# Performance work log

Hardware: AMD Instinct MI355X
Metric: run time of the kernel (lower is better)

Reference implementation:

```python
import jax, jax.numpy as jnp
import numpy as np

N_DATA = 1200000
FEAT = 128
BATCH = 512
N_NEG = 4096
TEMP = 0.07
MOMENTUM = 0.5


def _l2norm(x):
    return x / jnp.maximum(jnp.linalg.norm(x, axis=-1, keepdims=True), 1e-12)


def setup_inputs() -> dict:
    key = jax.random.key(0)
    k1, k2, k3, k4, k5 = jax.random.split(key, 5)
    negatives = _l2norm(jax.random.normal(k1, (N_DATA, FEAT), dtype=jnp.float32))
    return {
        "student_feat": jax.random.normal(k2, (BATCH, FEAT), dtype=jnp.float32),
        "teacher_feat": jax.random.normal(k3, (BATCH, FEAT), dtype=jnp.float32),
        "negatives": negatives,
        "indices": jax.random.randint(k4, (BATCH,), 0, N_DATA, dtype=jnp.int64)
            if jax.config.read("jax_enable_x64") else jax.random.randint(k4, (BATCH,), 0, N_DATA, dtype=jnp.int32),
        "neg_indices": jax.random.randint(k5, (BATCH, N_NEG), 0, N_DATA, dtype=jnp.int32),
    }


def reference(student_feat, teacher_feat, negatives, indices, neg_indices):
    s = _l2norm(student_feat)                       # [B, D]
    t = _l2norm(teacher_feat)                       # [B, D]
    pos_sim = jnp.sum(s * t, axis=1) / TEMP         # [B]
    neg_feat = negatives[neg_indices]               # [B, K, D] gather from bank
    neg_sim = jnp.einsum('bd,bkd->bk', s, neg_feat) / TEMP  # [B, K]
    logits = jnp.concatenate([pos_sim[:, None], neg_sim], axis=1)  # [B, 1+K]
    # cross-entropy with label 0 for every row
    loss = jnp.mean(jax.nn.logsumexp(logits, axis=1) - logits[:, 0])
    # EMA scatter update + renormalize of touched rows (no-grad side effect)
    upd = MOMENTUM * negatives[indices] + (1.0 - MOMENTUM) * t
    upd = _l2norm(upd)
    new_negatives = negatives.at[indices].set(upd)
    return loss, new_negatives
```

## Files before the change

### kernel.cpp

```cpp
#include <hip/hip_runtime.h>

constexpr int   FEAT   = 128;
constexpr int   BATCH  = 512;
constexpr int   NNEG   = 4096;
constexpr long  NDATA  = 1200000;
constexpr int   CHUNKS = 8;
constexpr int   NCOPY  = 1024;
constexpr long  NSRCG  = NDATA * FEAT / 4;
constexpr long  GMAXO  = NSRCG;
constexpr float INV_TEMP = 14.285714285714286f;
constexpr float LOG2E    = 1.4426950408889634f;
constexpr float LN2      = 0.6931471805599453f;
constexpr float K1       = INV_TEMP * LOG2E;

typedef float f4 __attribute__((ext_vector_type(4)));

__global__ __launch_bounds__(128) void prep_kernel(
    const float* __restrict__ sf, const float* __restrict__ tf,
    float* __restrict__ s_n, float* __restrict__ t_n, float* __restrict__ pos) {
  const int b = blockIdx.x, t = threadIdx.x;
  const float sv = sf[b * FEAT + t];
  const float tv = tf[b * FEAT + t];
  float ss = sv * sv, tt = tv * tv, st = sv * tv;
#pragma unroll
  for (int m = 1; m < 64; m <<= 1) {
    ss += __shfl_xor(ss, m);
    tt += __shfl_xor(tt, m);
    st += __shfl_xor(st, m);
  }
  __shared__ float sh[6];
  if ((t & 63) == 0) {
    const int w = t >> 6;
    sh[w * 3 + 0] = ss; sh[w * 3 + 1] = tt; sh[w * 3 + 2] = st;
  }
  __syncthreads();
  ss = sh[0] + sh[3]; tt = sh[1] + sh[4]; st = sh[2] + sh[5];
  const float snorm = fmaxf(sqrtf(ss), 1e-12f);
  const float tnorm = fmaxf(sqrtf(tt), 1e-12f);
  s_n[b * FEAT + t] = sv / snorm;
  t_n[b * FEAT + t] = tv / tnorm;
  if (t == 0) pos[b] = st / (snorm * tnorm) * INV_TEMP;
}

__global__ __launch_bounds__(256) void work_kernel(
    const float* __restrict__ neg, const int* __restrict__ nidx,
    const float* __restrict__ s_n, float* __restrict__ sumexp,
    float* __restrict__ out) {
  if (blockIdx.x < NCOPY) {
    const long n = NDATA * (long)FEAT;
    const f4* __restrict__ ps = (const f4*)neg;
    f4* __restrict__ po = (f4*)out;
    if (blockIdx.x == 0 && threadIdx.x == 0) {
      out[1] = neg[0]; out[2] = neg[1]; out[3] = neg[2];
      out[n] = neg[n - 1];
    }
    const int lane = threadIdx.x & 63;
    const int wid  = blockIdx.x * 4 + (threadIdx.x >> 6);
    constexpr long NWAVE = (long)NCOPY * 4;
    constexpr long PER   = (GMAXO - 1 + NWAVE - 1) / NWAVE;
    long base = 1 + (long)wid * PER;
    const long gend = (base + PER < GMAXO) ? base + PER : GMAXO;
    if (base >= gend) return;
    long src = base - 1 + lane;
    f4 cur = ps[src < NSRCG ? src : NSRCG - 1];
    while (base < gend) {
      const long nbase = base + 63;
      f4 nxt = {0.f, 0.f, 0.f, 0.f};
      if (nbase < gend) {
        const long ns = nbase - 1 + lane;
        nxt = ps[ns < NSRCG ? ns : NSRCG - 1];
      }
      const float pw = __shfl_up(cur.w, 1);
      const long g = base + lane - 1;
      if (lane >= 1 && g < gend) {
        f4 v; v.x = pw; v.y = cur.x; v.z = cur.y; v.w = cur.z;
        __builtin_nontemporal_store(v, po + g);
      }
      cur = nxt;
      base = nbase;
    }
    return;
  }
  __shared__ float part[4];
  const int blk   = blockIdx.x - NCOPY;
  const int b     = blk >> 3;
  const int chunk = blk & (CHUNKS - 1);
  const int t     = threadIdx.x;
  const int lane  = t & 63;
  const int w     = t >> 6;
  const int half  = lane >> 5;
  const int fo    = (lane & 31) * 4;
  const f4 s4 = *(const f4*)(s_n + b * FEAT + fo);
  const int kbase = b * NNEG + chunk * (NNEG / CHUNKS) + w * 128;
  float acc = 0.f;
  int off[8];
#pragma unroll
  for (int u = 0; u < 8; ++u)
    off[u] = nidx[kbase + 2 * u + half] * FEAT;
  for (int k0 = 0; k0 < 128; k0 += 16) {
    int noff[8];
    if (k0 + 16 < 128) {
#pragma unroll
      for (int u = 0; u < 8; ++u)
        noff[u] = nidx[kbase + k0 + 16 + 2 * u + half] * FEAT;
    }
    f4 v[8];
#pragma unroll
    for (int u = 0; u < 8; ++u)
      v[u] = *(const f4*)(neg + (long)off[u] + fo);
    float p[8];
#pragma unroll
    for (int u = 0; u < 8; ++u) {
      const f4 m = v[u] * s4;
      p[u] = (m.x + m.y) + (m.z + m.w);
    }
#pragma unroll
    for (int ms = 1; ms <= 16; ms <<= 1) {
#pragma unroll
      for (int u = 0; u < 8; ++u) p[u] += __shfl_xor(p[u], ms);
    }
#pragma unroll
    for (int u = 0; u < 8; ++u) acc += exp2f(fmaf(p[u], K1, -K1));
#pragma unroll
    for (int u = 0; u < 8; ++u) off[u] = noff[u];
  }
  acc *= (1.0f / 32.0f);
#pragma unroll
  for (int m = 1; m < 64; m <<= 1) acc += __shfl_xor(acc, m);
  if (lane == 0) part[w] = acc;
  __syncthreads();
  if (t == 0)
    sumexp[blk] = part[0] + part[1] + part[2] + part[3];
}

__global__ __launch_bounds__(256) void finish_kernel(
    const float* __restrict__ pos, const float* __restrict__ sumexp,
    const float* __restrict__ neg, const float* __restrict__ t_n,
    const int* __restrict__ indices, float* __restrict__ out) {
  const int t = threadIdx.x;
  if (blockIdx.x == 0) {
    float lsum = 0.f;
#pragma unroll
    for (int r = t; r < BATCH; r += 256) {
      const float p = pos[r];
      float tot = exp2f(fmaf(p, LOG2E, -K1));
#pragma unroll
      for (int c = 0; c < CHUNKS; ++c) tot += sumexp[r * CHUNKS + c];
      lsum += INV_TEMP + log2f(tot) * LN2 - p;
    }
#pragma unroll
    for (int m = 1; m < 64; m <<= 1) lsum += __shfl_xor(lsum, m);
    __shared__ float sh[4];
    if ((t & 63) == 0) sh[t >> 6] = lsum;
    __syncthreads();
    if (t == 0) out[0] = (sh[0] + sh[1] + sh[2] + sh[3]) / (float)BATCH;
    return;
  }
  const int b = blockIdx.x - 1;
  float* dst = out + 1;
  __shared__ int sidx[BATCH];
  __shared__ int flag;
  if (t == 0) flag = 0;
  for (int j = t; j < BATCH; j += 256) sidx[j] = indices[j];
  __syncthreads();
  const int idx = sidx[b];
  int later = 0;
  for (int j = t; j < BATCH; j += 256)
    if (j > b && sidx[j] == idx) later = 1;
  if (later) flag = 1;
  __syncthreads();
  if (flag) return;
  float u = 0.f, uu = 0.f;
  if (t < FEAT) {
    u = 0.5f * neg[(long)idx * FEAT + t] + 0.5f * t_n[b * FEAT + t];
    uu = u * u;
  }
#pragma unroll
  for (int m = 1; m < 64; m <<= 1) uu += __shfl_xor(uu, m);
  __shared__ float sh2[2];
  if (t == 0 || t == 64) sh2[t >> 6] = uu;
  __syncthreads();
  if (t < FEAT) {
    const float nrm = fmaxf(sqrtf(sh2[0] + sh2[1]), 1e-12f);
    dst[(long)idx * FEAT + t] = u / nrm;
  }
}

extern "C" void kernel_launch(void* const* d_in, const int* in_sizes, int n_in,
                              void* d_out, int out_size, void* d_ws, size_t ws_size,
                              hipStream_t stream) {
  const float* student   = (const float*)d_in[0];
  const float* teacher   = (const float*)d_in[1];
  const float* negatives = (const float*)d_in[2];
  const int*   indices   = (const int*)d_in[3];
  const int*   neg_idx   = (const int*)d_in[4];
  float* out = (float*)d_out;

  float* ws     = (float*)d_ws;
  float* s_n    = ws;
  float* t_n    = s_n + BATCH * FEAT;
  float* pos    = t_n + BATCH * FEAT;
  float* sumexp = pos + BATCH;

  prep_kernel<<<BATCH, 128, 0, stream>>>(student, teacher, s_n, t_n, pos);
  work_kernel<<<NCOPY + BATCH * CHUNKS, 256, 0, stream>>>(
      negatives, neg_idx, s_n, sumexp, out);
  finish_kernel<<<1 + BATCH, 256, 0, stream>>>(
      pos, sumexp, negatives, t_n, indices, out);
}
```

Before: 398.6 us.

## Split bank copy from gather kernel into separate copy and update launches

The full bank copy was previously co-scheduled with the gathered negative-similarity blocks in one launch. It now runs in its own kernel after the similarity kernel, alongside the loss reduction, with twice as many copy blocks. The EMA row update moves to a separate 128-thread kernel launched afterwards. This removes contention between the streaming copy and the random gathers, at the cost of serialising the two phases and adding one extra launch.

```diff
diff --git a/kernel.cpp b/kernel.cpp
--- a/kernel.cpp
+++ b/kernel.cpp
@@ -5,7 +5,7 @@
 constexpr int   NNEG   = 4096;
 constexpr long  NDATA  = 1200000;
 constexpr int   CHUNKS = 8;
-constexpr int   NCOPY  = 1024;
+constexpr int   NCOPYB = 2048;
 constexpr long  NSRCG  = NDATA * FEAT / 4;
 constexpr long  GMAXO  = NSRCG;
 constexpr float INV_TEMP = 14.285714285714286f;
@@ -42,47 +42,11 @@
   if (t == 0) pos[b] = st / (snorm * tnorm) * INV_TEMP;
 }
 
-__global__ __launch_bounds__(256) void work_kernel(
+__global__ __launch_bounds__(256) void negsim_kernel(
     const float* __restrict__ neg, const int* __restrict__ nidx,
-    const float* __restrict__ s_n, float* __restrict__ sumexp,
-    float* __restrict__ out) {
-  if (blockIdx.x < NCOPY) {
-    const long n = NDATA * (long)FEAT;
-    const f4* __restrict__ ps = (const f4*)neg;
-    f4* __restrict__ po = (f4*)out;
-    if (blockIdx.x == 0 && threadIdx.x == 0) {
-      out[1] = neg[0]; out[2] = neg[1]; out[3] = neg[2];
-      out[n] = neg[n - 1];
-    }
-    const int lane = threadIdx.x & 63;
-    const int wid  = blockIdx.x * 4 + (threadIdx.x >> 6);
-    constexpr long NWAVE = (long)NCOPY * 4;
-    constexpr long PER   = (GMAXO - 1 + NWAVE - 1) / NWAVE;
-    long base = 1 + (long)wid * PER;
-    const long gend = (base + PER < GMAXO) ? base + PER : GMAXO;
-    if (base >= gend) return;
-    long src = base - 1 + lane;
-    f4 cur = ps[src < NSRCG ? src : NSRCG - 1];
-    while (base < gend) {
-      const long nbase = base + 63;
-      f4 nxt = {0.f, 0.f, 0.f, 0.f};
-      if (nbase < gend) {
-        const long ns = nbase - 1 + lane;
-        nxt = ps[ns < NSRCG ? ns : NSRCG - 1];
-      }
-      const float pw = __shfl_up(cur.w, 1);
-      const long g = base + lane - 1;
-      if (lane >= 1 && g < gend) {
-        f4 v; v.x = pw; v.y = cur.x; v.z = cur.y; v.w = cur.z;
-        __builtin_nontemporal_store(v, po + g);
-      }
-      cur = nxt;
-      base = nbase;
-    }
-    return;
-  }
+    const float* __restrict__ s_n, float* __restrict__ sumexp) {
   __shared__ float part[4];
-  const int blk   = blockIdx.x - NCOPY;
+  const int blk   = blockIdx.x;
   const int b     = blk >> 3;
   const int chunk = blk & (CHUNKS - 1);
   const int t     = threadIdx.x;
@@ -133,10 +97,9 @@
     sumexp[blk] = part[0] + part[1] + part[2] + part[3];
 }
 
-__global__ __launch_bounds__(256) void finish_kernel(
-    const float* __restrict__ pos, const float* __restrict__ sumexp,
-    const float* __restrict__ neg, const float* __restrict__ t_n,
-    const int* __restrict__ indices, float* __restrict__ out) {
+__global__ __launch_bounds__(256) void copyloss_kernel(
+    const float* __restrict__ neg, const float* __restrict__ pos,
+    const float* __restrict__ sumexp, float* __restrict__ out) {
   const int t = threadIdx.x;
   if (blockIdx.x == 0) {
     float lsum = 0.f;
@@ -153,37 +116,68 @@
     __shared__ float sh[4];
     if ((t & 63) == 0) sh[t >> 6] = lsum;
     __syncthreads();
-    if (t == 0) out[0] = (sh[0] + sh[1] + sh[2] + sh[3]) / (float)BATCH;
+    if (t == 0) {
+      out[0] = (sh[0] + sh[1] + sh[2] + sh[3]) / (float)BATCH;
+      const long n = NDATA * (long)FEAT;
+      out[1] = neg[0]; out[2] = neg[1]; out[3] = neg[2];
+      out[n] = neg[n - 1];
+    }
     return;
   }
-  const int b = blockIdx.x - 1;
-  float* dst = out + 1;
+  const f4* __restrict__ ps = (const f4*)neg;
+  f4* __restrict__ po = (f4*)out;
+  const int lane = t & 63;
+  const int wid  = (blockIdx.x - 1) * 4 + (t >> 6);
+  constexpr long NWAVE = (long)NCOPYB * 4;
+  constexpr long PER   = (GMAXO - 1 + NWAVE - 1) / NWAVE;
+  long base = 1 + (long)wid * PER;
+  const long gend = (base + PER < GMAXO) ? base + PER : GMAXO;
+  if (base >= gend) return;
+  long src = base - 1 + lane;
+  f4 cur = ps[src < NSRCG ? src : NSRCG - 1];
+  while (base < gend) {
+    const long nbase = base + 63;
+    f4 nxt = {0.f, 0.f, 0.f, 0.f};
+    if (nbase < gend) {
+      const long ns = nbase - 1 + lane;
+      nxt = ps[ns < NSRCG ? ns : NSRCG - 1];
+    }
+    const float pw = __shfl_up(cur.w, 1);
+    const long g = base + lane - 1;
+    if (lane >= 1 && g < gend) {
+      f4 v; v.x = pw; v.y = cur.x; v.z = cur.y; v.w = cur.z;
+      __builtin_nontemporal_store(v, po + g);
+    }
+    cur = nxt;
+    base = nbase;
+  }
+}
+
+__global__ __launch_bounds__(128) void update_kernel(
+    const float* __restrict__ neg, const float* __restrict__ t_n,
+    const int* __restrict__ indices, float* __restrict__ dst) {
+  const int b = blockIdx.x, t = threadIdx.x;
   __shared__ int sidx[BATCH];
   __shared__ int flag;
   if (t == 0) flag = 0;
-  for (int j = t; j < BATCH; j += 256) sidx[j] = indices[j];
+  for (int j = t; j < BATCH; j += 128) sidx[j] = indices[j];
   __syncthreads();
   const int idx = sidx[b];
   int later = 0;
-  for (int j = t; j < BATCH; j += 256)
+  for (int j = t; j < BATCH; j += 128)
     if (j > b && sidx[j] == idx) later = 1;
   if (later) flag = 1;
   __syncthreads();
   if (flag) return;
-  float u = 0.f, uu = 0.f;
-  if (t < FEAT) {
-    u = 0.5f * neg[(long)idx * FEAT + t] + 0.5f * t_n[b * FEAT + t];
-    uu = u * u;
-  }
+  const float u = 0.5f * neg[(long)idx * FEAT + t] + 0.5f * t_n[b * FEAT + t];
+  float uu = u * u;
 #pragma unroll
   for (int m = 1; m < 64; m <<= 1) uu += __shfl_xor(uu, m);
   __shared__ float sh2[2];
-  if (t == 0 || t == 64) sh2[t >> 6] = uu;
-  __syncthreads();
-  if (t < FEAT) {
-    const float nrm = fmaxf(sqrtf(sh2[0] + sh2[1]), 1e-12f);
-    dst[(long)idx * FEAT + t] = u / nrm;
-  }
+  if ((t & 63) == 0) sh2[t >> 6] = uu;
+  __syncthreads();
+  const float nrm = fmaxf(sqrtf(sh2[0] + sh2[1]), 1e-12f);
+  dst[(long)idx * FEAT + t] = u / nrm;
 }
 
 extern "C" void kernel_launch(void* const* d_in, const int* in_sizes, int n_in,
@@ -203,8 +197,7 @@
   float* sumexp = pos + BATCH;
 
   prep_kernel<<<BATCH, 128, 0, stream>>>(student, teacher, s_n, t_n, pos);
-  work_kernel<<<NCOPY + BATCH * CHUNKS, 256, 0, stream>>>(
-      negatives, neg_idx, s_n, sumexp, out);
-  finish_kernel<<<1 + BATCH, 256, 0, stream>>>(
-      pos, sumexp, negatives, t_n, indices, out);
-}
+  negsim_kernel<<<BATCH * CHUNKS, 256, 0, stream>>>(negatives, neg_idx, s_n, sumexp);
+  copyloss_kernel<<<1 + NCOPYB, 256, 0, stream>>>(negatives, pos, sumexp, out);
+  update_kernel<<<BATCH, 128, 0, stream>>>(negatives, t_n, indices, out + 1);
+}
```

Measured after the change: 446.5 us. +12.0%, slower.
